# Kernel optimization log

Hardware: AMD Instinct MI355X
Metric: run time of the kernel (lower is better)

Reference implementation:

```python
import jax, jax.numpy as jnp
import numpy as np

S = 2048      # sequence length (q_seq == kv_seq, self-attention)
D = 1024      # hidden_size
H = 16        # num_heads
DH = D // H   # per-head dim
LN_EPS = 1e-5


def setup_inputs() -> dict:
    key = jax.random.key(0)
    ks = jax.random.split(key, 8)
    init = lambda k, shape: (jax.random.normal(k, shape, dtype=jnp.float32)
                             / np.float32(np.sqrt(shape[-1])))
    return {
        "x": jax.random.normal(ks[0], (S, D), dtype=jnp.float32),
        "logit_bias": jax.random.normal(ks[1], (S, H * S), dtype=jnp.float32) * 0.1,
        "mask": jax.random.bernoulli(ks[2], 0.9, (S, S)),
        "Wq": init(ks[3], (D, D)),
        "Wk": init(ks[4], (D, D)),
        "Wv": init(ks[5], (D, D)),
        "Wo": init(ks[6], (D, D)),
        "ln_w": jnp.ones((D,), dtype=jnp.float32),
        "ln_b": jnp.zeros((D,), dtype=jnp.float32),
    }


def reference(x, logit_bias, mask, Wq, Wk, Wv, Wo, ln_w, ln_b):
    # Projections (eqx.nn.Linear: y = W @ x, no bias), split into heads.
    q = (x @ Wq.T).reshape(S, H, DH)  # [s,h,d]
    k = (x @ Wk.T).reshape(S, H, DH)  # [S,h,d]
    v = (x @ Wv.T).reshape(S, H, DH)  # [S,h,d]

    # Scaled scores + per-head additive logit bias.
    scale = jnp.asarray(1.0 / np.sqrt(DH), dtype=q.dtype)
    logits = jnp.einsum('shd,Shd->hsS', q * scale, k)  # [h,s,S]
    logits = logits + logit_bias.reshape(S, H, S).transpose(1, 0, 2)

    # Boolean mask (q_seq, kv_seq) broadcast over heads.
    logits = jnp.where(mask[None, :, :], logits, jnp.finfo(logits.dtype).min)

    # Stable softmax in float32 (matches result_type promotion in source).
    weights = jax.nn.softmax(logits.astype(jnp.float32), axis=-1).astype(logits.dtype)

    attn = jnp.einsum('hsS,Shd->shd', weights, v).reshape(S, D)
    attn_out = attn @ Wo.T  # output projection, no bias

    # Residual + LayerNorm over last dim (eqx.nn.LayerNorm, eps=1e-5).
    res = attn_out + x
    mean = jnp.mean(res, axis=-1, keepdims=True)
    var = jnp.var(res, axis=-1, keepdims=True)
    normed = (res - mean) * jax.lax.rsqrt(var + LN_EPS)
    return normed * ln_w + ln_b
```

## Files before the change

kernel.cpp:

```cpp
#include <hip/hip_runtime.h>

#define SS 2048
#define DD 1024
#define HH 16
#define DHD 64
#define HSN (HH * SS)
#define LOG2E 1.44269504088896340736f

typedef __bf16 bf16x8 __attribute__((ext_vector_type(8)));
typedef __bf16 bf16x4 __attribute__((ext_vector_type(4)));
typedef float f32x4 __attribute__((ext_vector_type(4)));
typedef unsigned int u32;
typedef unsigned long long u64;

__device__ __forceinline__ void glds16(const void* g, void* l) {
  __builtin_amdgcn_global_load_lds(
      (const __attribute__((address_space(1))) u32*)(const u32*)g,
      (__attribute__((address_space(3))) u32*)(u32*)l, 16, 0, 0);
}

__global__ __launch_bounds__(256) void cvt_all_kernel(const float* __restrict__ x,
                                                      const float* __restrict__ Wq,
                                                      const float* __restrict__ Wk,
                                                      const float* __restrict__ Wv,
                                                      const float* __restrict__ Wo,
                                                      __bf16* xb, __bf16* Wqb, __bf16* Wkb,
                                                      __bf16* Wvb, __bf16* Wob) {
  const int z = blockIdx.z;
  const int n4 = (z == 0 ? SS * DD : DD * DD) / 4;
  const int i = blockIdx.x * 256 + threadIdx.x;
  if (i >= n4) return;
  const float* in = z == 0 ? x : (z == 1 ? Wq : (z == 2 ? Wk : (z == 3 ? Wv : Wo)));
  __bf16* out = z == 0 ? xb : (z == 1 ? Wqb : (z == 2 ? Wkb : (z == 3 ? Wvb : Wob)));
  const float4 v = ((const float4*)in)[i];
  bf16x4 r;
  r[0] = (__bf16)v.x; r[1] = (__bf16)v.y; r[2] = (__bf16)v.z; r[3] = (__bf16)v.w;
  *(bf16x4*)&out[(long)i * 4] = r;
}

__global__ __launch_bounds__(256) void pack_mask(const int* __restrict__ mask,
                                                 u64* __restrict__ mp) {
  const long i = (long)blockIdx.x * 256 + threadIdx.x;
  const u64 b = __ballot(mask[i] != 0);
  if ((threadIdx.x & 63) == 0) mp[i >> 6] = b;
}

template <int BM>
__device__ __forceinline__ void gemm_body(const __bf16* __restrict__ A,
                                          const __bf16* __restrict__ B,
                                          void* __restrict__ Cout, float scale, int mode,
                                          int bx, int by) {
  constexpr int MR = BM / 32;
  __shared__ alignas(16) __bf16 As[BM * 32];
  __shared__ alignas(16) __bf16 Bs[128 * 32];
  const int tid = threadIdx.x;
  const int lane = tid & 63;
  const int wave = tid >> 6;
  const long m0 = (long)by * BM;
  const long n0 = (long)bx * 128;
  const int wm = (wave >> 1) * (BM / 2);
  const int wn = (wave & 1) * 64;
  const int g = lane >> 4, r16 = lane & 15;
  const int srow = tid >> 2, sseg = (tid & 3) * 8;

  f32x4 acc[MR][4] = {};

  for (int k0 = 0; k0 < DD; k0 += 32) {
#pragma unroll
    for (int it = 0; it < 2; ++it) {
      const int row = srow + it * 64;
      glds16(&B[(n0 + row) * DD + k0 + sseg], &Bs[row * 32 + sseg]);
    }
#pragma unroll
    for (int it = 0; it < BM / 64; ++it) {
      const int row = srow + it * 64;
      glds16(&A[(m0 + row) * DD + k0 + sseg], &As[row * 32 + sseg]);
    }
    __syncthreads();
    bf16x8 af[MR], bfr[4];
#pragma unroll
    for (int r = 0; r < MR; ++r) af[r] = *(const bf16x8*)&As[(wm + r * 16 + r16) * 32 + g * 8];
#pragma unroll
    for (int c = 0; c < 4; ++c) bfr[c] = *(const bf16x8*)&Bs[(wn + c * 16 + r16) * 32 + g * 8];
#pragma unroll
    for (int r = 0; r < MR; ++r)
#pragma unroll
      for (int c = 0; c < 4; ++c)
        acc[r][c] = __builtin_amdgcn_mfma_f32_16x16x32_bf16(af[r], bfr[c], acc[r][c], 0, 0, 0);
    __syncthreads();
  }

  if (mode == 2) {
#pragma unroll
    for (int r = 0; r < MR; ++r)
#pragma unroll
      for (int c = 0; c < 4; ++c) {
        const long row0 = m0 + wm + r * 16 + g * 4;
        const long col = n0 + wn + c * 16 + r16;
        bf16x4 rv;
#pragma unroll
        for (int i = 0; i < 4; ++i) rv[i] = (__bf16)(acc[r][c][i] * scale);
        *(bf16x4*)&((__bf16*)Cout)[col * SS + row0] = rv;
      }
  } else {
#pragma unroll
    for (int r = 0; r < MR; ++r)
#pragma unroll
      for (int c = 0; c < 4; ++c)
#pragma unroll
        for (int i = 0; i < 4; ++i) {
          const long row = m0 + wm + r * 16 + g * 4 + i;
          const long col = n0 + wn + c * 16 + r16;
          const float v = acc[r][c][i] * scale;
          if (mode == 1) ((float*)Cout)[row * DD + col] = v;
          else           ((__bf16*)Cout)[row * DD + col] = (__bf16)v;
        }
  }
}

__global__ __launch_bounds__(256) void gemm_qkv(const __bf16* __restrict__ A,
                                                const __bf16* __restrict__ B0,
                                                const __bf16* __restrict__ B1,
                                                const __bf16* __restrict__ B2,
                                                __bf16* C0, __bf16* C1, __bf16* C2,
                                                float s0) {
  const int z = blockIdx.z;
  const __bf16* B = z == 0 ? B0 : (z == 1 ? B1 : B2);
  __bf16* C = z == 0 ? C0 : (z == 1 ? C1 : C2);
  gemm_body<64>(A, B, C, z == 0 ? s0 : 1.0f, z == 2 ? 2 : 0, blockIdx.x, blockIdx.y);
}

__global__ __launch_bounds__(256) void gemm_o(const __bf16* __restrict__ A,
                                              const __bf16* __restrict__ B,
                                              float* __restrict__ C) {
  gemm_body<64>(A, B, C, 1.0f, 1, blockIdx.x, blockIdx.y);
}

__global__ __launch_bounds__(256) void attn_kernel(
    const __bf16* __restrict__ Q, const __bf16* __restrict__ K,
    const __bf16* __restrict__ Vt, const float* __restrict__ bias,
    const u64* __restrict__ mp, __bf16* __restrict__ Aout) {
  __shared__ alignas(16) __bf16 Ks[64][72];
  __shared__ alignas(16) __bf16 Vts[64][72];
  __shared__ alignas(16) __bf16 Ps[4][16][72];
  const int tid = threadIdx.x;
  const int lane = tid & 63;
  const int wave = tid >> 6;
  const int h = blockIdx.y;
  const int q0 = blockIdx.x * 64 + wave * 16;
  const int g = lane >> 4, r16 = lane & 15;
  const int myq = q0 + r16;
  const int srow = tid >> 2;

  bf16x8 qf[2];
#pragma unroll
  for (int c = 0; c < 2; ++c)
    qf[c] = *(const bf16x8*)&Q[(long)myq * DD + h * DHD + c * 32 + g * 8];

  const float* bp = &bias[(long)myq * HSN + h * SS];
  const u64* mrow_p = &mp[(long)myq * (SS / 64)];

  f32x4 o[4] = {};
  float mrow = -__builtin_inff();
  float lsum = 0.f;

  for (int kv0 = 0; kv0 < SS; kv0 += 64) {
    __syncthreads();
#pragma unroll
    for (int it = 0; it < 2; ++it) {
      const int seg = (tid & 3) + it * 4;
      *(bf16x8*)&Ks[srow][seg * 8] =
          *(const bf16x8*)&K[(long)(kv0 + srow) * DD + h * DHD + seg * 8];
      *(bf16x8*)&Vts[srow][seg * 8] =
          *(const bf16x8*)&Vt[(long)(h * DHD + srow) * SS + kv0 + seg * 8];
    }

    float4 bv[4];
#pragma unroll
    for (int t = 0; t < 4; ++t) bv[t] = *(const float4*)&bp[kv0 + t * 16 + g * 4];
    const u64 mw = mrow_p[kv0 >> 6];
    __syncthreads();

    f32x4 s[4];
#pragma unroll
    for (int t = 0; t < 4; ++t) {
      bf16x8 kf0 = *(const bf16x8*)&Ks[t * 16 + r16][g * 8];
      bf16x8 kf1 = *(const bf16x8*)&Ks[t * 16 + r16][32 + g * 8];
      f32x4 acc = {};
      acc = __builtin_amdgcn_mfma_f32_16x16x32_bf16(kf0, qf[0], acc, 0, 0, 0);
      s[t] = __builtin_amdgcn_mfma_f32_16x16x32_bf16(kf1, qf[1], acc, 0, 0, 0);
    }

    float sv[4][4];
#pragma unroll
    for (int t = 0; t < 4; ++t) {
      const u32 mb = (u32)(mw >> (t * 16 + g * 4));
      sv[t][0] = (mb & 1u) ? s[t][0] + bv[t].x * LOG2E : -1e38f;
      sv[t][1] = (mb & 2u) ? s[t][1] + bv[t].y * LOG2E : -1e38f;
      sv[t][2] = (mb & 4u) ? s[t][2] + bv[t].z * LOG2E : -1e38f;
      sv[t][3] = (mb & 8u) ? s[t][3] + bv[t].w * LOG2E : -1e38f;
    }

    float m4 = -1e38f;
#pragma unroll
    for (int t = 0; t < 4; ++t)
#pragma unroll
      for (int i = 0; i < 4; ++i) m4 = fmaxf(m4, sv[t][i]);
    m4 = fmaxf(m4, __shfl_xor(m4, 16));
    m4 = fmaxf(m4, __shfl_xor(m4, 32));
    const float mnew = fmaxf(mrow, m4);
    const float alpha = exp2f(mrow - mnew);
    float ps = 0.f;
    float p[4][4];
#pragma unroll
    for (int t = 0; t < 4; ++t)
#pragma unroll
      for (int i = 0; i < 4; ++i) {
        p[t][i] = exp2f(sv[t][i] - mnew);
        ps += p[t][i];
      }
    ps += __shfl_xor(ps, 16);
    ps += __shfl_xor(ps, 32);
    lsum = lsum * alpha + ps;
    mrow = mnew;
#pragma unroll
    for (int db = 0; db < 4; ++db) o[db] *= alpha;

#pragma unroll
    for (int t = 0; t < 4; ++t) {
      bf16x4 pb;
#pragma unroll
      for (int i = 0; i < 4; ++i) pb[i] = (__bf16)p[t][i];
      *(bf16x4*)&Ps[wave][r16][t * 16 + g * 4] = pb;
    }

#pragma unroll
    for (int kh = 0; kh < 2; ++kh) {
      bf16x8 pf = *(const bf16x8*)&Ps[wave][r16][kh * 32 + g * 8];
#pragma unroll
      for (int db = 0; db < 4; ++db) {
        bf16x8 vf = *(const bf16x8*)&Vts[db * 16 + r16][kh * 32 + g * 8];
        o[db] = __builtin_amdgcn_mfma_f32_16x16x32_bf16(vf, pf, o[db], 0, 0, 0);
      }
    }
  }

  const float rn = 1.f / lsum;
#pragma unroll
  for (int db = 0; db < 4; ++db) {
    bf16x4 r;
#pragma unroll
    for (int i = 0; i < 4; ++i) r[i] = (__bf16)(o[db][i] * rn);
    *(bf16x4*)&Aout[(long)myq * DD + h * DHD + db * 16 + g * 4] = r;
  }
}

__global__ __launch_bounds__(256) void ln_kernel(const float* __restrict__ attn_out,
                                                 const float* __restrict__ x,
                                                 const float* __restrict__ w,
                                                 const float* __restrict__ b,
                                                 float* __restrict__ out) {
  const long row = blockIdx.x;
  const int tid = threadIdx.x;
  const float4 a4 = ((const float4*)&attn_out[row * DD])[tid];
  const float4 x4 = ((const float4*)&x[row * DD])[tid];
  float v[4] = {a4.x + x4.x, a4.y + x4.y, a4.z + x4.z, a4.w + x4.w};
  float s = 0.f, s2 = 0.f;
#pragma unroll
  for (int j = 0; j < 4; ++j) { s += v[j]; s2 += v[j] * v[j]; }
#pragma unroll
  for (int off = 1; off < 64; off <<= 1) {
    s  += __shfl_xor(s, off);
    s2 += __shfl_xor(s2, off);
  }
  __shared__ float ss[4], ss2[4];
  if ((tid & 63) == 0) { ss[tid >> 6] = s; ss2[tid >> 6] = s2; }
  __syncthreads();
  s = ss[0] + ss[1] + ss[2] + ss[3];
  s2 = ss2[0] + ss2[1] + ss2[2] + ss2[3];
  const float mean = s * (1.f / DD);
  const float var = s2 * (1.f / DD) - mean * mean;
  const float inv = rsqrtf(var + 1e-5f);
  const float4 w4 = ((const float4*)w)[tid];
  const float4 b4 = ((const float4*)b)[tid];
  float4 o4;
  o4.x = (v[0] - mean) * inv * w4.x + b4.x;
  o4.y = (v[1] - mean) * inv * w4.y + b4.y;
  o4.z = (v[2] - mean) * inv * w4.z + b4.z;
  o4.w = (v[3] - mean) * inv * w4.w + b4.w;
  ((float4*)&out[row * DD])[tid] = o4;
}

extern "C" void kernel_launch(void* const* d_in, const int* in_sizes, int n_in,
                              void* d_out, int out_size, void* d_ws, size_t ws_size,
                              hipStream_t stream) {
  const float* x    = (const float*)d_in[0];
  const float* bias = (const float*)d_in[1];
  const int*   mask = (const int*)d_in[2];
  const float* Wq   = (const float*)d_in[3];
  const float* Wk   = (const float*)d_in[4];
  const float* Wv   = (const float*)d_in[5];
  const float* Wo   = (const float*)d_in[6];
  const float* lnw  = (const float*)d_in[7];
  const float* lnb  = (const float*)d_in[8];
  float* out = (float*)d_out;

  char* ws = (char*)d_ws;
  const size_t MB = 1024 * 1024;
  __bf16* xb   = (__bf16*)(ws + 0);
  __bf16* Wqb  = (__bf16*)(ws + 4 * MB);
  __bf16* Wkb  = (__bf16*)(ws + 6 * MB);
  __bf16* Wvb  = (__bf16*)(ws + 8 * MB);
  __bf16* Wob  = (__bf16*)(ws + 10 * MB);
  __bf16* Qb   = (__bf16*)(ws + 12 * MB);
  __bf16* Kb   = (__bf16*)(ws + 16 * MB);
  __bf16* Vtb  = (__bf16*)(ws + 24 * MB);
  __bf16* Atnb = (__bf16*)(ws + 28 * MB);
  float*  AOut = (float*)(ws + 32 * MB);
  u64*    mpk  = (u64*)(ws + 40 * MB);

  cvt_all_kernel<<<dim3(SS * DD / 1024, 1, 5), dim3(256), 0, stream>>>(
      x, Wq, Wk, Wv, Wo, xb, Wqb, Wkb, Wvb, Wob);

  pack_mask<<<dim3(SS * SS / 256), dim3(256), 0, stream>>>(mask, mpk);

  gemm_qkv<<<dim3(DD / 128, SS / 64, 3), dim3(256), 0, stream>>>(
      xb, Wqb, Wkb, Wvb, Qb, Kb, Vtb, 0.125f * LOG2E);

  attn_kernel<<<dim3(SS / 64, HH), dim3(256), 0, stream>>>(Qb, Kb, Vtb, bias, mpk, Atnb);

  gemm_o<<<dim3(DD / 128, SS / 64), dim3(256), 0, stream>>>(Atnb, Wob, AOut);

  ln_kernel<<<dim3(SS), dim3(256), 0, stream>>>(AOut, x, lnw, lnb, out);
}
```

Before: 487.4 us.

## Double-buffer attention K/V loads, fuse mask packing and residual add

The attention loop now prefetches the next K/V tile, bias and mask into registers while computing on the current LDS buffer. LDS is ping-ponged between two buffers so one barrier per tile replaces two, aiming to hide global load latency behind the MFMA and softmax work. Mask packing is folded into the conversion kernel as an extra grid slice, removing one launch. The residual add moves into the output GEMM epilogue, so the LayerNorm kernel reads one array instead of two. Register pressure rises from the prefetch registers, and the tail iteration issues redundant loads from tile 0.

Result: no change. 482.0 us (-1.1%).

```diff
diff --git a/kernel.cpp b/kernel.cpp
--- a/kernel.cpp
+++ b/kernel.cpp
@@ -25,8 +25,21 @@
                                                       const float* __restrict__ Wv,
                                                       const float* __restrict__ Wo,
                                                       __bf16* xb, __bf16* Wqb, __bf16* Wkb,
-                                                      __bf16* Wvb, __bf16* Wob) {
+                                                      __bf16* Wvb, __bf16* Wob,
+                                                      const int* __restrict__ mask,
+                                                      u64* __restrict__ mp) {
   const int z = blockIdx.z;
+  if (z == 5) {
+    const int wid = (blockIdx.x * 256 + threadIdx.x) >> 6;
+    const int lane = threadIdx.x & 63;
+#pragma unroll
+    for (int w = 0; w < 8; ++w) {
+      const long word = (long)wid * 8 + w;
+      const u64 b = __ballot(mask[word * 64 + lane] != 0);
+      if (lane == 0) mp[word] = b;
+    }
+    return;
+  }
   const int n4 = (z == 0 ? SS * DD : DD * DD) / 4;
   const int i = blockIdx.x * 256 + threadIdx.x;
   if (i >= n4) return;
@@ -38,18 +51,12 @@
   *(bf16x4*)&out[(long)i * 4] = r;
 }
 
-__global__ __launch_bounds__(256) void pack_mask(const int* __restrict__ mask,
-                                                 u64* __restrict__ mp) {
-  const long i = (long)blockIdx.x * 256 + threadIdx.x;
-  const u64 b = __ballot(mask[i] != 0);
-  if ((threadIdx.x & 63) == 0) mp[i >> 6] = b;
-}
-
 template <int BM>
 __device__ __forceinline__ void gemm_body(const __bf16* __restrict__ A,
                                           const __bf16* __restrict__ B,
                                           void* __restrict__ Cout, float scale, int mode,
-                                          int bx, int by) {
+                                          int bx, int by,
+                                          const float* __restrict__ Xres = nullptr) {
   constexpr int MR = BM / 32;
   __shared__ alignas(16) __bf16 As[BM * 32];
   __shared__ alignas(16) __bf16 Bs[128 * 32];
@@ -111,8 +118,9 @@
         for (int i = 0; i < 4; ++i) {
           const long row = m0 + wm + r * 16 + g * 4 + i;
           const long col = n0 + wn + c * 16 + r16;
-          const float v = acc[r][c][i] * scale;
-          if (mode == 1) ((float*)Cout)[row * DD + col] = v;
+          float v = acc[r][c][i] * scale;
+          if (mode == 3) v += Xres[row * DD + col];
+          if (mode != 0) ((float*)Cout)[row * DD + col] = v;
           else           ((__bf16*)Cout)[row * DD + col] = (__bf16)v;
         }
   }
@@ -132,16 +140,17 @@
 
 __global__ __launch_bounds__(256) void gemm_o(const __bf16* __restrict__ A,
                                               const __bf16* __restrict__ B,
-                                              float* __restrict__ C) {
-  gemm_body<64>(A, B, C, 1.0f, 1, blockIdx.x, blockIdx.y);
+                                              float* __restrict__ C,
+                                              const float* __restrict__ x) {
+  gemm_body<64>(A, B, C, 1.0f, 3, blockIdx.x, blockIdx.y, x);
 }
 
 __global__ __launch_bounds__(256) void attn_kernel(
     const __bf16* __restrict__ Q, const __bf16* __restrict__ K,
     const __bf16* __restrict__ Vt, const float* __restrict__ bias,
     const u64* __restrict__ mp, __bf16* __restrict__ Aout) {
-  __shared__ alignas(16) __bf16 Ks[64][72];
-  __shared__ alignas(16) __bf16 Vts[64][72];
+  __shared__ alignas(16) __bf16 Ks[2][64][72];
+  __shared__ alignas(16) __bf16 Vts[2][64][72];
   __shared__ alignas(16) __bf16 Ps[4][16][72];
   const int tid = threadIdx.x;
   const int lane = tid & 63;
@@ -164,33 +173,42 @@
   float mrow = -__builtin_inff();
   float lsum = 0.f;
 
-  for (int kv0 = 0; kv0 < SS; kv0 += 64) {
-    __syncthreads();
+  bf16x8 kA[2], vA[2], kB[2], vB[2];
+  float4 bvA[4], bvB[4];
+  u64 mwA, mwB;
+
+  auto loadKV = [&](int kv0, bf16x8 (&kr)[2], bf16x8 (&vr)[2]) {
 #pragma unroll
     for (int it = 0; it < 2; ++it) {
       const int seg = (tid & 3) + it * 4;
-      *(bf16x8*)&Ks[srow][seg * 8] =
-          *(const bf16x8*)&K[(long)(kv0 + srow) * DD + h * DHD + seg * 8];
-      *(bf16x8*)&Vts[srow][seg * 8] =
-          *(const bf16x8*)&Vt[(long)(h * DHD + srow) * SS + kv0 + seg * 8];
-    }
-
-    float4 bv[4];
+      kr[it] = *(const bf16x8*)&K[(long)(kv0 + srow) * DD + h * DHD + seg * 8];
+      vr[it] = *(const bf16x8*)&Vt[(long)(h * DHD + srow) * SS + kv0 + seg * 8];
+    }
+  };
+  auto loadBM = [&](int kv0, float4 (&bv)[4], u64& mw) {
 #pragma unroll
     for (int t = 0; t < 4; ++t) bv[t] = *(const float4*)&bp[kv0 + t * 16 + g * 4];
-    const u64 mw = mrow_p[kv0 >> 6];
-    __syncthreads();
-
+    mw = mrow_p[kv0 >> 6];
+  };
+  auto writeLDS = [&](int buf, const bf16x8 (&kr)[2], const bf16x8 (&vr)[2]) {
+#pragma unroll
+    for (int it = 0; it < 2; ++it) {
+      const int seg8 = ((tid & 3) + it * 4) * 8;
+      *(bf16x8*)&Ks[buf][srow][seg8] = kr[it];
+      *(bf16x8*)&Vts[buf][srow][seg8] = vr[it];
+    }
+  };
+
+  auto compute = [&](int buf, const float4 (&bv)[4], u64 mw) {
     f32x4 s[4];
 #pragma unroll
     for (int t = 0; t < 4; ++t) {
-      bf16x8 kf0 = *(const bf16x8*)&Ks[t * 16 + r16][g * 8];
-      bf16x8 kf1 = *(const bf16x8*)&Ks[t * 16 + r16][32 + g * 8];
+      bf16x8 kf0 = *(const bf16x8*)&Ks[buf][t * 16 + r16][g * 8];
+      bf16x8 kf1 = *(const bf16x8*)&Ks[buf][t * 16 + r16][32 + g * 8];
       f32x4 acc = {};
       acc = __builtin_amdgcn_mfma_f32_16x16x32_bf16(kf0, qf[0], acc, 0, 0, 0);
       s[t] = __builtin_amdgcn_mfma_f32_16x16x32_bf16(kf1, qf[1], acc, 0, 0, 0);
     }
-
     float sv[4][4];
 #pragma unroll
     for (int t = 0; t < 4; ++t) {
@@ -200,7 +218,6 @@
       sv[t][2] = (mb & 4u) ? s[t][2] + bv[t].z * LOG2E : -1e38f;
       sv[t][3] = (mb & 8u) ? s[t][3] + bv[t].w * LOG2E : -1e38f;
     }
-
     float m4 = -1e38f;
 #pragma unroll
     for (int t = 0; t < 4; ++t)
@@ -225,7 +242,6 @@
     mrow = mnew;
 #pragma unroll
     for (int db = 0; db < 4; ++db) o[db] *= alpha;
-
 #pragma unroll
     for (int t = 0; t < 4; ++t) {
       bf16x4 pb;
@@ -233,16 +249,41 @@
       for (int i = 0; i < 4; ++i) pb[i] = (__bf16)p[t][i];
       *(bf16x4*)&Ps[wave][r16][t * 16 + g * 4] = pb;
     }
-
 #pragma unroll
     for (int kh = 0; kh < 2; ++kh) {
       bf16x8 pf = *(const bf16x8*)&Ps[wave][r16][kh * 32 + g * 8];
 #pragma unroll
       for (int db = 0; db < 4; ++db) {
-        bf16x8 vf = *(const bf16x8*)&Vts[db * 16 + r16][kh * 32 + g * 8];
+        bf16x8 vf = *(const bf16x8*)&Vts[buf][db * 16 + r16][kh * 32 + g * 8];
         o[db] = __builtin_amdgcn_mfma_f32_16x16x32_bf16(vf, pf, o[db], 0, 0, 0);
       }
     }
+  };
+
+  loadKV(0, kA, vA);
+  loadBM(0, bvA, mwA);
+  writeLDS(0, kA, vA);
+  loadKV(64, kB, vB);
+  loadBM(64, bvB, mwB);
+  __syncthreads();
+
+  for (int t2 = 0; t2 < SS; t2 += 128) {
+    compute(0, bvA, mwA);
+    writeLDS(1, kB, vB);
+    {
+      const int kvn = (t2 + 128 < SS) ? t2 + 128 : 0;
+      loadKV(kvn, kA, vA);
+      loadBM(kvn, bvA, mwA);
+    }
+    __syncthreads();
+    compute(1, bvB, mwB);
+    writeLDS(0, kA, vA);
+    {
+      const int kvn = (t2 + 192 < SS) ? t2 + 192 : 0;
+      loadKV(kvn, kB, vB);
+      loadBM(kvn, bvB, mwB);
+    }
+    __syncthreads();
   }
 
   const float rn = 1.f / lsum;
@@ -255,16 +296,14 @@
   }
 }
 
-__global__ __launch_bounds__(256) void ln_kernel(const float* __restrict__ attn_out,
-                                                 const float* __restrict__ x,
+__global__ __launch_bounds__(256) void ln_kernel(const float* __restrict__ res,
                                                  const float* __restrict__ w,
                                                  const float* __restrict__ b,
                                                  float* __restrict__ out) {
   const long row = blockIdx.x;
   const int tid = threadIdx.x;
-  const float4 a4 = ((const float4*)&attn_out[row * DD])[tid];
-  const float4 x4 = ((const float4*)&x[row * DD])[tid];
-  float v[4] = {a4.x + x4.x, a4.y + x4.y, a4.z + x4.z, a4.w + x4.w};
+  const float4 a4 = ((const float4*)&res[row * DD])[tid];
+  float v[4] = {a4.x, a4.y, a4.z, a4.w};
   float s = 0.f, s2 = 0.f;
 #pragma unroll
   for (int j = 0; j < 4; ++j) { s += v[j]; s2 += v[j] * v[j]; }
@@ -319,17 +358,15 @@
   float*  AOut = (float*)(ws + 32 * MB);
   u64*    mpk  = (u64*)(ws + 40 * MB);
 
-  cvt_all_kernel<<<dim3(SS * DD / 1024, 1, 5), dim3(256), 0, stream>>>(
-      x, Wq, Wk, Wv, Wo, xb, Wqb, Wkb, Wvb, Wob);
-
-  pack_mask<<<dim3(SS * SS / 256), dim3(256), 0, stream>>>(mask, mpk);
+  cvt_all_kernel<<<dim3(SS * DD / 1024, 1, 6), dim3(256), 0, stream>>>(
+      x, Wq, Wk, Wv, Wo, xb, Wqb, Wkb, Wvb, Wob, mask, mpk);
 
   gemm_qkv<<<dim3(DD / 128, SS / 64, 3), dim3(256), 0, stream>>>(
       xb, Wqb, Wkb, Wvb, Qb, Kb, Vtb, 0.125f * LOG2E);
 
   attn_kernel<<<dim3(SS / 64, HH), dim3(256), 0, stream>>>(Qb, Kb, Vtb, bias, mpk, Atnb);
 
-  gemm_o<<<dim3(DD / 128, SS / 64), dim3(256), 0, stream>>>(Atnb, Wob, AOut);
-
-  ln_kernel<<<dim3(SS), dim3(256), 0, stream>>>(AOut, x, lnw, lnb, out);
-}
+  gemm_o<<<dim3(DD / 128, SS / 64), dim3(256), 0, stream>>>(Atnb, Wob, AOut, x);
+
+  ln_kernel<<<dim3(SS), dim3(256), 0, stream>>>(AOut, lnw, lnb, out);
+}
```
